# Kernel tuning notes

Hardware: AMD Instinct MI355X
Metric: run time of the kernel (lower is better)

Reference implementation:

```python
import jax, jax.numpy as jnp
import numpy as np

D_MODEL = 768
D_STATE = 16
D_CONV = 4
EXPAND = 2
D_INNER = EXPAND * D_MODEL  # 1536
DT_RANK = -(-D_MODEL // 16)  # ceil(768/16) = 48
BATCH = 1
SEQ = 2048


def _silu(v):
    return v * jax.nn.sigmoid(v)


def setup_inputs() -> dict:
    key = jax.random.key(0)
    ks = jax.random.split(key, 8)
    s = 0.02
    x = jax.random.normal(ks[0], (BATCH, SEQ, D_MODEL), jnp.float32)
    in_proj_w = jax.random.normal(ks[1], (2 * D_INNER, D_MODEL), jnp.float32) * s
    conv_w = jax.random.normal(ks[2], (D_INNER, 1, D_CONV), jnp.float32) * s  # depthwise, groups=D_INNER
    conv_b = jnp.zeros((D_INNER,), jnp.float32)
    x_proj_w = jax.random.normal(ks[3], (DT_RANK + 2 * D_STATE, D_INNER), jnp.float32) * s
    dt_proj_w = jax.random.normal(ks[4], (D_INNER, DT_RANK), jnp.float32) * s
    dt_proj_b = jax.random.normal(ks[5], (D_INNER,), jnp.float32) * 0.01
    # A = repeat_interleave(arange(1, d_state+1), d_inner rows); A_log = log(A)
    A_log = jnp.log(jnp.tile(jnp.arange(1, D_STATE + 1, dtype=jnp.float32)[None, :], (D_INNER, 1)))
    D = jnp.ones((D_INNER,), jnp.float32)
    out_proj_w = jax.random.normal(ks[6], (D_MODEL, D_INNER), jnp.float32) * s
    return {"x": x, "in_proj_w": in_proj_w, "conv_w": conv_w, "conv_b": conv_b,
            "x_proj_w": x_proj_w, "dt_proj_w": dt_proj_w, "dt_proj_b": dt_proj_b,
            "A_log": A_log, "D": D, "out_proj_w": out_proj_w}


def reference(x, in_proj_w, conv_w, conv_b, x_proj_w, dt_proj_w, dt_proj_b, A_log, D, out_proj_w):
    b, L, d = x.shape
    # in_proj then split into x-branch and gate z
    xz = x @ in_proj_w.T                       # (b, L, 2*d_inner)
    xh, z = jnp.split(xz, 2, axis=-1)          # each (b, L, d_inner)
    # causal depthwise conv1d: torch pads d_conv-1 both sides then slices [:L];
    # equivalent to left-pad d_conv-1, right-pad 0
    xc = jnp.transpose(xh, (0, 2, 1))          # (b, d_inner, L)
    xc = jax.lax.conv_general_dilated(
        xc, conv_w, window_strides=(1,), padding=[(D_CONV - 1, 0)],
        feature_group_count=D_INNER, dimension_numbers=("NCH", "OIH", "NCH"))
    xc = xc + conv_b[None, :, None]
    u = _silu(jnp.transpose(xc, (0, 2, 1)))    # (b, L, d_inner)
    # input-dependent dt, B, C
    x_dbl = u @ x_proj_w.T                     # (b, L, dt_rank + 2*d_state)
    dt, Bm, Cm = jnp.split(x_dbl, [DT_RANK, DT_RANK + D_STATE], axis=-1)
    dt = jax.nn.softplus(dt @ dt_proj_w.T + dt_proj_b)  # (b, L, d_inner)
    A = -jnp.exp(A_log)                        # (d_inner, d_state)
    # selective scan via cumprod/cumsum (faithful to source math)
    dA = jnp.exp(dt[..., None] * A[None, None])              # (b, L, d_inner, d_state)
    dBu = dt[..., None] * Bm[:, :, None, :] * u[..., None]   # (b, L, d_inner, d_state)
    p = jnp.cumprod(dA, axis=1)
    eps = jnp.finfo(u.dtype).eps
    p_safe = jnp.maximum(p, eps)
    g = jnp.cumsum(dBu / p_safe, axis=1)
    h = g * p
    y = jnp.sum(h * Cm[:, :, None, :], axis=-1) + D * u      # (b, L, d_inner)
    y = y * _silu(z)
    return y @ out_proj_w.T                    # (b, L, d_model); dropout=identity (eval)
```

## Files before the change

kernel.cpp:

```cpp
#include <hip/hip_runtime.h>
#include <hip/hip_bf16.h>

#define LSEQ 2048
#define DMODEL 768
#define DINNER 1536
#define DSTATE 16
#define DTRANK 48
#define XDBL_W (DTRANK + 2*DSTATE)
#define CHUNK 32
#define NCHUNK (LSEQ / CHUNK)
#define NDN (DINNER * DSTATE)
#define FEPS 1.1920928955078125e-07f
#define SPLITK 8
#define OSPLIT 4
#define LDST2 36

typedef short bf16x8 __attribute__((ext_vector_type(8)));
typedef float f32x4 __attribute__((ext_vector_type(4)));
typedef unsigned short u16;

__device__ __forceinline__ u16 f2bf_rn(float f) {
    unsigned u = __float_as_uint(f);
    unsigned r = u + 0x7FFFu + ((u >> 16) & 1u);
    return (u16)(r >> 16);
}
__device__ __forceinline__ float bf2f(u16 h) {
    return __uint_as_float(((unsigned)h) << 16);
}

template<int CTRL>
__device__ __forceinline__ float qperm(float x) {
    return __int_as_float(__builtin_amdgcn_update_dpp(
        0, __float_as_int(x), CTRL, 0xF, 0xF, true));
}

__global__ __launch_bounds__(256) void cvt_all(
    const float* __restrict__ w_in,  u16* __restrict__ wihi, u16* __restrict__ wilo, int n1,
    const float* __restrict__ w_out, u16* __restrict__ owhi, u16* __restrict__ owlo, int n2,
    const float* __restrict__ x,     u16* __restrict__ xhi,  u16* __restrict__ xlo)
{
    int i4 = (blockIdx.x * 256 + threadIdx.x) * 4;
    const float* src; u16* hi; u16* lo; int off;
    if (i4 < n1)            { src = w_in;  hi = wihi; lo = wilo; off = i4; }
    else if (i4 < n1 + n2)  { src = w_out; hi = owhi; lo = owlo; off = i4 - n1; }
    else                    { src = x;     hi = xhi;  lo = xlo;  off = i4 - n1 - n2; }
    float4 v = *(const float4*)&src[off];
    u16 h0 = f2bf_rn(v.x), h1 = f2bf_rn(v.y), h2 = f2bf_rn(v.z), h3 = f2bf_rn(v.w);
    u16 l0 = f2bf_rn(v.x - bf2f(h0));
    u16 l1 = f2bf_rn(v.y - bf2f(h1));
    u16 l2 = f2bf_rn(v.z - bf2f(h2));
    u16 l3 = f2bf_rn(v.w - bf2f(h3));
    *(ushort4*)&hi[off] = make_ushort4(h0, h1, h2, h3);
    *(ushort4*)&lo[off] = make_ushort4(l0, l1, l2, l3);
}

template<int BN>
__global__ __launch_bounds__(256) void mfma_gemm_tn(
    const u16* __restrict__ Ahi, const u16* __restrict__ Alo,
    const u16* __restrict__ Bhi, const u16* __restrict__ Blo,
    float* __restrict__ C, int ldc, int ldk, int Klen)
{
    constexpr int BUFSZ = 8192 + BN * 64;
    constexpr int NJ = BN / 32;
    __shared__ u16 lds[2 * BUFSZ];
    const int tid = threadIdx.x;
    const int wid = tid >> 6;
    const int lane = tid & 63;

    int nwg = gridDim.x * gridDim.y * gridDim.z;
    int lin = (blockIdx.z * gridDim.y + blockIdx.y) * gridDim.x + blockIdx.x;
    int q = nwg >> 3;
    int swz = (lin & 7) * q + (lin >> 3);
    int bx = swz % gridDim.x;
    int tmp = swz / gridDim.x;
    int by = tmp % gridDim.y;
    int bz = tmp / gridDim.y;

    const int m0 = bx * 128;
    const int n0 = by * BN;
    const int Koff = bz * Klen;

    const int st_subrow = lane >> 2;
    const int st_cphys = lane & 3;
    const u16* myplane = (wid == 0) ? Ahi : (wid == 1) ? Alo : (wid == 2) ? Bhi : Blo;
    const int rowbase = (wid < 2) ? m0 : n0;
    const int nIss = (wid < 2) ? 8 : (BN / 16);
    const int planeOff = (wid < 2) ? wid * 4096 : 8192 + (wid - 2) * (BN * 32);

    f32x4 acc[4][NJ] = {};
    const int wm = (wid >> 1) * 64;
    const int wn = (wid & 1) * (BN / 2);
    const int fr = lane & 15;
    const int fc = lane >> 4;
    const int nsteps = Klen / 32;

    auto stage = [&](int buf, int k0) {
#pragma unroll
        for (int j = 0; j < 8; ++j) {
            if (j < nIss) {
                int row = j * 16 + st_subrow;
                int clog = st_cphys ^ ((row >> 1) & 3);
                const u16* g = myplane + (size_t)(rowbase + row) * ldk + k0 + clog * 8;
                u16* l = &lds[buf * BUFSZ + planeOff + j * 512];
                __builtin_amdgcn_global_load_lds(
                    (const __attribute__((address_space(1))) unsigned int*)g,
                    (__attribute__((address_space(3))) unsigned int*)l, 16, 0, 0);
            }
        }
    };

    stage(0, Koff);
    int cur = 0;
    for (int t = 0; t < nsteps; ++t) {
        __syncthreads();
        if (t + 1 < nsteps) stage(cur ^ 1, Koff + (t + 1) * 32);

        bf16x8 ah[4], al[4], bh[NJ], bl[NJ];
        const bf16x8* L = (const bf16x8*)&lds[cur * BUFSZ];
#pragma unroll
        for (int mi = 0; mi < 4; ++mi) {
            int r = wm + mi * 16 + fr;
            int idx = r * 4 + (fc ^ ((r >> 1) & 3));
            ah[mi] = L[idx];
            al[mi] = L[512 + idx];
        }
#pragma unroll
        for (int nj = 0; nj < NJ; ++nj) {
            int r = wn + nj * 16 + fr;
            int idx = r * 4 + (fc ^ ((r >> 1) & 3));
            bh[nj] = L[1024 + idx];
            bl[nj] = L[1024 + BN * 4 + idx];
        }
#pragma unroll
        for (int mi = 0; mi < 4; ++mi)
#pragma unroll
            for (int nj = 0; nj < NJ; ++nj) {
                acc[mi][nj] = __builtin_amdgcn_mfma_f32_16x16x32_bf16(ah[mi], bh[nj], acc[mi][nj], 0, 0, 0);
                acc[mi][nj] = __builtin_amdgcn_mfma_f32_16x16x32_bf16(ah[mi], bl[nj], acc[mi][nj], 0, 0, 0);
                acc[mi][nj] = __builtin_amdgcn_mfma_f32_16x16x32_bf16(al[mi], bh[nj], acc[mi][nj], 0, 0, 0);
            }
        cur ^= 1;
    }

    float* Cz = C + (size_t)bz * LSEQ * ldc;
#pragma unroll
    for (int mi = 0; mi < 4; ++mi) {
        int row_b = m0 + wm + mi * 16 + (lane >> 4) * 4;
#pragma unroll
        for (int nj = 0; nj < NJ; ++nj) {
            int col = n0 + wn + nj * 16 + (lane & 15);
#pragma unroll
            for (int r = 0; r < 4; ++r)
                Cz[(size_t)(row_b + r) * ldc + col] = acc[mi][nj][r];
        }
    }
}

__global__ __launch_bounds__(256) void reduce4(
    const float* __restrict__ Ppart, float* __restrict__ out, int n)
{
    int i = (blockIdx.x * 256 + threadIdx.x) * 4;
    if (i >= n) return;
    float4 a0 = *(const float4*)&Ppart[i];
    float4 a1 = *(const float4*)&Ppart[(size_t)n + i];
    float4 a2 = *(const float4*)&Ppart[(size_t)2 * n + i];
    float4 a3 = *(const float4*)&Ppart[(size_t)3 * n + i];
    float4 r;
    r.x = ((a0.x + a1.x) + a2.x) + a3.x;
    r.y = ((a0.y + a1.y) + a2.y) + a3.y;
    r.z = ((a0.z + a1.z) + a2.z) + a3.z;
    r.w = ((a0.w + a1.w) + a2.w) + a3.w;
    *(float4*)&out[i] = r;
}

template<int EPI>
__global__ __launch_bounds__(256) void gemm_tn(
    const float* __restrict__ A, int lda,
    const float* __restrict__ B, int ldb,
    float* __restrict__ C, int ldc,
    int M, int N, int K,
    const float* __restrict__ bias)
{
    __shared__ float As[16][64 + 4];
    __shared__ float Bs[16][64 + 4];
    const int tid = threadIdx.x;
    const int m0 = blockIdx.x * 64;
    const int n0 = blockIdx.y * 64;
    const int tx = tid & 15;
    const int ty = tid >> 4;
    const int lr = tid >> 4;
    const int lc = tid & 15;
    float acc[4][4] = {};

    for (int k0 = 0; k0 < K; k0 += 16) {
        const int k = k0 + lc;
#pragma unroll
        for (int i = 0; i < 4; ++i) {
            int m = m0 + lr + i * 16;
            As[lc][lr + i * 16] = (m < M) ? A[(size_t)m * lda + k] : 0.f;
        }
#pragma unroll
        for (int i = 0; i < 4; ++i) {
            int n = n0 + lr + i * 16;
            Bs[lc][lr + i * 16] = (n < N) ? B[(size_t)n * ldb + k] : 0.f;
        }
        __syncthreads();
#pragma unroll
        for (int kk = 0; kk < 16; ++kk) {
            float a[4], b[4];
#pragma unroll
            for (int i = 0; i < 4; ++i) a[i] = As[kk][ty * 4 + i];
#pragma unroll
            for (int j = 0; j < 4; ++j) b[j] = Bs[kk][tx * 4 + j];
#pragma unroll
            for (int i = 0; i < 4; ++i)
#pragma unroll
                for (int j = 0; j < 4; ++j)
                    acc[i][j] = fmaf(a[i], b[j], acc[i][j]);
        }
        __syncthreads();
    }

#pragma unroll
    for (int i = 0; i < 4; ++i) {
        int m = m0 + ty * 4 + i;
        if (m >= M) continue;
#pragma unroll
        for (int j = 0; j < 4; ++j) {
            int n = n0 + tx * 4 + j;
            if (n >= N) continue;
            float v = acc[i][j];
            if (EPI == 1) {
                v += bias[n];
                v = fmaxf(v, 0.f) + log1pf(expf(-fabsf(v)));
            }
            C[(size_t)m * ldc + n] = v;
        }
    }
}

__global__ __launch_bounds__(256) void gemm_tn_splitk(
    const float* __restrict__ A, int lda,
    const float* __restrict__ B, int ldb,
    float* __restrict__ Cpart, int ldc,
    int M, int N, int Kchunk)
{
    __shared__ float As[16][64 + 4];
    __shared__ float Bs[16][64 + 4];
    const int tid = threadIdx.x;
    const int m0 = blockIdx.x * 64;
    const int n0 = blockIdx.y * 64;
    const int kb = blockIdx.z * Kchunk;
    const int tx = tid & 15;
    const int ty = tid >> 4;
    const int lr = tid >> 4;
    const int lc = tid & 15;
    float acc[4][4] = {};

    for (int k0 = kb; k0 < kb + Kchunk; k0 += 16) {
        const int k = k0 + lc;
#pragma unroll
        for (int i = 0; i < 4; ++i) {
            int m = m0 + lr + i * 16;
            As[lc][lr + i * 16] = (m < M) ? A[(size_t)m * lda + k] : 0.f;
        }
#pragma unroll
        for (int i = 0; i < 4; ++i) {
            int n = n0 + lr + i * 16;
            Bs[lc][lr + i * 16] = (n < N) ? B[(size_t)n * ldb + k] : 0.f;
        }
        __syncthreads();
#pragma unroll
        for (int kk = 0; kk < 16; ++kk) {
            float a[4], b[4];
#pragma unroll
            for (int i = 0; i < 4; ++i) a[i] = As[kk][ty * 4 + i];
#pragma unroll
            for (int j = 0; j < 4; ++j) b[j] = Bs[kk][tx * 4 + j];
#pragma unroll
            for (int i = 0; i < 4; ++i)
#pragma unroll
                for (int j = 0; j < 4; ++j)
                    acc[i][j] = fmaf(a[i], b[j], acc[i][j]);
        }
        __syncthreads();
    }

    float* Cs = Cpart + (size_t)blockIdx.z * M * ldc;
#pragma unroll
    for (int i = 0; i < 4; ++i) {
        int m = m0 + ty * 4 + i;
        if (m >= M) continue;
#pragma unroll
        for (int j = 0; j < 4; ++j) {
            int n = n0 + tx * 4 + j;
            if (n >= N) continue;
            Cs[(size_t)m * ldc + n] = acc[i][j];
        }
    }
}

__global__ __launch_bounds__(256) void splitk_reduce(
    const float* __restrict__ Ppart, float* __restrict__ out, int n)
{
    int i = blockIdx.x * 256 + threadIdx.x;
    if (i >= n) return;
    float s = 0.f;
#pragma unroll
    for (int z = 0; z < SPLITK; ++z) s += Ppart[(size_t)z * n + i];
    out[i] = s;
}

__global__ __launch_bounds__(256) void conv_silu_kernel(
    const float* __restrict__ xz,
    const float* __restrict__ conv_w,
    const float* __restrict__ conv_b,
    float* __restrict__ u)
{
    int idx = blockIdx.x * 256 + threadIdx.x;
    int d = idx % DINNER;
    int t0 = (idx / DINNER) * 4;
    float w[4];
#pragma unroll
    for (int j = 0; j < 4; ++j) w[j] = conv_w[d * 4 + j];
    const float b = conv_b[d];
    float xv[7];
#pragma unroll
    for (int k = 0; k < 7; ++k) {
        int s = t0 - 3 + k;
        xv[k] = (s >= 0) ? xz[(size_t)s * (2 * DINNER) + d] : 0.f;
    }
#pragma unroll
    for (int i = 0; i < 4; ++i) {
        float acc = b;
#pragma unroll
        for (int j = 0; j < 4; ++j)
            acc = fmaf(xv[i + j], w[j], acc);
        float sig = 1.f / (1.f + __expf(-acc));
        u[(size_t)(t0 + i) * DINNER + d] = acc * sig;
    }
}

__global__ __launch_bounds__(256) void dt_chunksum(
    const float* __restrict__ dtm, float* __restrict__ csum)
{
    int d = blockIdx.x * 256 + threadIdx.x;
    int c = blockIdx.y;
    size_t base = (size_t)c * CHUNK * DINNER + d;
    float s = 0.f;
#pragma unroll
    for (int i = 0; i < CHUNK; ++i)
        s += dtm[base + (size_t)i * DINNER];
    csum[(size_t)c * DINNER + d] = s;
}

__global__ __launch_bounds__(256) void cumdt_excl(float* __restrict__ csum)
{
    int d = blockIdx.x * 256 + threadIdx.x;
    float v[NCHUNK];
#pragma unroll
    for (int c = 0; c < NCHUNK; ++c)
        v[c] = csum[(size_t)c * DINNER + d];
    float run = 0.f;
#pragma unroll
    for (int c = 0; c < NCHUNK; ++c) {
        float t = v[c];
        v[c] = run;
        run += t;
    }
#pragma unroll
    for (int c = 0; c < NCHUNK; ++c)
        csum[(size_t)c * DINNER + d] = v[c];
}

template<int PROD>
__global__ __launch_bounds__(256) void scan_exclusive(float* __restrict__ buf)
{
    const int dn = blockIdx.x * 256 + threadIdx.x;
    float v[NCHUNK];
#pragma unroll
    for (int c = 0; c < NCHUNK; ++c)
        v[c] = buf[(size_t)c * NDN + dn];
    float run = PROD ? 1.f : 0.f;
#pragma unroll
    for (int c = 0; c < NCHUNK; ++c) {
        float t = v[c];
        v[c] = run;
        run = PROD ? run * t : run + t;
    }
#pragma unroll
    for (int c = 0; c < NCHUNK; ++c)
        buf[(size_t)c * NDN + dn] = v[c];
}

__global__ __launch_bounds__(256) void scan_chunksum(
    const float* __restrict__ dtm,
    const float* __restrict__ u,
    const float* __restrict__ xdbl,
    const float* __restrict__ A_log,
    const float* __restrict__ cumdt,
    float* __restrict__ S)
{
    __shared__ float sdtT[16][LDST2], sduT[16][LDST2], sBT[16][LDST2];
    const int tid = threadIdx.x;
    const int d0 = blockIdx.x * 16;
    const int t0 = blockIdx.y * CHUNK;
    const int r = tid >> 4, c = tid & 15;
#pragma unroll
    for (int i = 0; i < 2; ++i) {
        int t = r + i * 16;
        size_t row = (size_t)(t0 + t);
        float dtv = dtm[row * DINNER + d0 + c];
        sdtT[c][t] = dtv;
        sduT[c][t] = dtv * u[row * DINNER + d0 + c];
        sBT[c][t]  = xdbl[row * XDBL_W + DTRANK + c];
    }
    __syncthreads();
    const int n = tid & 15, dl = tid >> 4;
    const float Acoef = -expf(A_log[(d0 + dl) * DSTATE + n]);
    float s = cumdt[(size_t)blockIdx.y * DINNER + d0 + dl];
    float acc = 0.f;
#pragma unroll
    for (int tb = 0; tb < CHUNK / 4; ++tb) {
        f32x4 dq  = *(const f32x4*)&sdtT[dl][tb * 4];
        f32x4 duq = *(const f32x4*)&sduT[dl][tb * 4];
        f32x4 bq  = *(const f32x4*)&sBT[n][tb * 4];
#pragma unroll
        for (int j = 0; j < 4; ++j) {
            s += dq[j];
            float p = __expf(Acoef * s);
            acc += __fdividef(duq[j] * bq[j], fmaxf(p, FEPS));
        }
    }
    S[(size_t)blockIdx.y * NDN + d0 * DSTATE + tid] = acc;
}

__global__ __launch_bounds__(256) void scan_final(
    const float* __restrict__ dtm,
    const float* __restrict__ u,
    const float* __restrict__ xdbl,
    const float* __restrict__ A_log,
    const float* __restrict__ cumdt,
    const float* __restrict__ Gpre,
    float* __restrict__ xz)
{
    __shared__ float sdtT[64][LDST2], sduT[64][LDST2];
    __shared__ float sBT[16][LDST2], sCT[16][LDST2];
    const int tid = threadIdx.x;
    const int d0 = blockIdx.x * 64;
    const int t0 = blockIdx.y * CHUNK;

#pragma unroll
    for (int i = 0; i < 8; ++i) {
        int idx = i * 256 + tid;
        int dl = idx & 63, tl = idx >> 6;
        size_t row = (size_t)(t0 + tl);
        float dtv = dtm[row * DINNER + d0 + dl];
        sdtT[dl][tl] = dtv;
        sduT[dl][tl] = dtv * u[row * DINNER + d0 + dl];
    }
#pragma unroll
    for (int i = 0; i < 2; ++i) {
        int idx = i * 256 + tid;
        int n = idx & 15, tl = idx >> 4;
        size_t row = (size_t)(t0 + tl);
        sBT[n][tl] = xdbl[row * XDBL_W + DTRANK + n];
        sCT[n][tl] = xdbl[row * XDBL_W + DTRANK + DSTATE + n];
    }
    __syncthreads();

    const int lane = tid & 63, wid = tid >> 6;
    const int dloc = wid * 16 + (lane >> 2);
    const int d = d0 + dloc;
    const int nq = lane & 3;

    f32x4 Ar = *(const f32x4*)&A_log[d * DSTATE + nq * 4];
    float Ac[4] = {-expf(Ar[0]), -expf(Ar[1]), -expf(Ar[2]), -expf(Ar[3])};
    size_t pgbase = (size_t)blockIdx.y * NDN + (size_t)d * DSTATE + nq * 4;
    f32x4 g = *(const f32x4*)&Gpre[pgbase];
    float s = cumdt[(size_t)blockIdx.y * DINNER + d];

#pragma unroll
    for (int tb = 0; tb < CHUNK / 4; ++tb) {
        f32x4 dq  = *(const f32x4*)&sdtT[dloc][tb * 4];
        f32x4 duq = *(const f32x4*)&sduT[dloc][tb * 4];
        f32x4 b0 = *(const f32x4*)&sBT[nq * 4 + 0][tb * 4];
        f32x4 b1 = *(const f32x4*)&sBT[nq * 4 + 1][tb * 4];
        f32x4 b2 = *(const f32x4*)&sBT[nq * 4 + 2][tb * 4];
        f32x4 b3 = *(const f32x4*)&sBT[nq * 4 + 3][tb * 4];
        f32x4 c0 = *(const f32x4*)&sCT[nq * 4 + 0][tb * 4];
        f32x4 c1 = *(const f32x4*)&sCT[nq * 4 + 1][tb * 4];
        f32x4 c2 = *(const f32x4*)&sCT[nq * 4 + 2][tb * 4];
        f32x4 c3 = *(const f32x4*)&sCT[nq * 4 + 3][tb * 4];
#pragma unroll
        for (int j = 0; j < 4; ++j) {
            float duv = duq[j];
            s += dq[j];
            float p0 = __expf(Ac[0] * s);
            float p1 = __expf(Ac[1] * s);
            float p2 = __expf(Ac[2] * s);
            float p3 = __expf(Ac[3] * s);
            g[0] += __fdividef(duv * b0[j], fmaxf(p0, FEPS));
            g[1] += __fdividef(duv * b1[j], fmaxf(p1, FEPS));
            g[2] += __fdividef(duv * b2[j], fmaxf(p2, FEPS));
            g[3] += __fdividef(duv * b3[j], fmaxf(p3, FEPS));
            float part = (g[0] * p0) * c0[j];
            part = fmaf(g[1] * p1, c1[j], part);
            part = fmaf(g[2] * p2, c2[j], part);
            part = fmaf(g[3] * p3, c3[j], part);
            part += qperm<0xB1>(part);
            part += qperm<0x4E>(part);
            if (nq == 0)
                xz[(size_t)(t0 + tb * 4 + j) * (2 * DINNER) + d] = part;
        }
    }
}

__global__ __launch_bounds__(256) void gate_kernel(
    const float* __restrict__ xz,
    const float* __restrict__ u,
    const float* __restrict__ Dvec,
    u16* __restrict__ yhi, u16* __restrict__ ylo)
{
    int i4 = (blockIdx.x * 256 + threadIdx.x) * 4;
    if (i4 >= LSEQ * DINNER) return;
    int t = i4 / DINNER;
    int d = i4 - t * DINNER;
    size_t base = (size_t)t * (2 * DINNER) + d;
    float4 part = *(const float4*)&xz[base];
    float4 zv   = *(const float4*)&xz[base + DINNER];
    float4 uv   = *(const float4*)&u[i4];
    float4 Dd   = *(const float4*)&Dvec[d];
    float pa[4] = {part.x, part.y, part.z, part.w};
    float za[4] = {zv.x, zv.y, zv.z, zv.w};
    float ua[4] = {uv.x, uv.y, uv.z, uv.w};
    float Da[4] = {Dd.x, Dd.y, Dd.z, Dd.w};
    u16 ha[4], la[4];
#pragma unroll
    for (int j = 0; j < 4; ++j) {
        float sig = 1.f / (1.f + __expf(-za[j]));
        float yv = (pa[j] + Da[j] * ua[j]) * (za[j] * sig);
        ha[j] = f2bf_rn(yv);
        la[j] = f2bf_rn(yv - bf2f(ha[j]));
    }
    *(ushort4*)&yhi[i4] = make_ushort4(ha[0], ha[1], ha[2], ha[3]);
    *(ushort4*)&ylo[i4] = make_ushort4(la[0], la[1], la[2], la[3]);
}

extern "C" void kernel_launch(void* const* d_in, const int* in_sizes, int n_in,
                              void* d_out, int out_size, void* d_ws, size_t ws_size,
                              hipStream_t stream) {
    const float* x          = (const float*)d_in[0];
    const float* in_proj_w  = (const float*)d_in[1];
    const float* conv_w     = (const float*)d_in[2];
    const float* conv_b     = (const float*)d_in[3];
    const float* x_proj_w   = (const float*)d_in[4];
    const float* dt_proj_w  = (const float*)d_in[5];
    const float* dt_proj_b  = (const float*)d_in[6];
    const float* A_log      = (const float*)d_in[7];
    const float* Dvec       = (const float*)d_in[8];
    const float* out_proj_w = (const float*)d_in[9];
    float* out = (float*)d_out;

    char* w = (char*)d_ws;
    auto alloc = [&](size_t bytes) { char* p = w; w += (bytes + 255) & ~(size_t)255; return p; };

    float* xz    = (float*)alloc((size_t)LSEQ * 2 * DINNER * 4);
    float* u     = (float*)alloc((size_t)LSEQ * DINNER * 4);
    float* xdbl  = (float*)alloc((size_t)LSEQ * XDBL_W * 4);
    float* dtb   = (float*)alloc((size_t)LSEQ * DINNER * 4);
    float* csum  = (float*)alloc((size_t)NCHUNK * DINNER * 4);
    float* S     = (float*)alloc((size_t)NCHUNK * NDN * 4);
    float* Ppart = (float*)alloc((size_t)SPLITK * LSEQ * XDBL_W * 4);
    u16* xhi  = (u16*)alloc((size_t)LSEQ * DMODEL * 2);
    u16* xlo  = (u16*)alloc((size_t)LSEQ * DMODEL * 2);
    u16* wihi = (u16*)alloc((size_t)2 * DINNER * DMODEL * 2);
    u16* wilo = (u16*)alloc((size_t)2 * DINNER * DMODEL * 2);
    u16* owhi = (u16*)alloc((size_t)DMODEL * DINNER * 2);
    u16* owlo = (u16*)alloc((size_t)DMODEL * DINNER * 2);
    u16* yhi  = (u16*)alloc((size_t)LSEQ * DINNER * 2);
    u16* ylo  = (u16*)alloc((size_t)LSEQ * DINNER * 2);
    float* opart = u;

    dim3 blk(256);

    {
        int n1 = 2 * DINNER * DMODEL;
        int n2 = DMODEL * DINNER;
        int n3 = LSEQ * DMODEL;
        cvt_all<<<(n1 + n2 + n3) / 1024, blk, 0, stream>>>(
            in_proj_w, wihi, wilo, n1, out_proj_w, owhi, owlo, n2, x, xhi, xlo);
    }

    mfma_gemm_tn<128><<<dim3(LSEQ / 128, (2 * DINNER) / 128, 1), blk, 0, stream>>>(
        xhi, xlo, wihi, wilo, xz, 2 * DINNER, DMODEL, DMODEL);

    conv_silu_kernel<<<(LSEQ / 4) * DINNER / 256, blk, 0, stream>>>(xz, conv_w, conv_b, u);

    gemm_tn_splitk<<<dim3(LSEQ / 64, (XDBL_W + 63) / 64, SPLITK), blk, 0, stream>>>(
        u, DINNER, x_proj_w, DINNER, Ppart, XDBL_W, LSEQ, XDBL_W, DINNER / SPLITK);
    splitk_reduce<<<(LSEQ * XDBL_W + 255) / 256, blk, 0, stream>>>(Ppart, xdbl, LSEQ * XDBL_W);

    gemm_tn<1><<<dim3(LSEQ / 64, DINNER / 64), blk, 0, stream>>>(
        xdbl, XDBL_W, dt_proj_w, DTRANK, dtb, DINNER, LSEQ, DINNER, DTRANK, dt_proj_b);

    dt_chunksum<<<dim3(DINNER / 256, NCHUNK), blk, 0, stream>>>(dtb, csum);
    cumdt_excl<<<DINNER / 256, blk, 0, stream>>>(csum);
    scan_chunksum<<<dim3(DINNER / 16, NCHUNK), blk, 0, stream>>>(dtb, u, xdbl, A_log, csum, S);
    scan_exclusive<0><<<NDN / 256, blk, 0, stream>>>(S);
    scan_final<<<dim3(DINNER / 64, NCHUNK), blk, 0, stream>>>(
        dtb, u, xdbl, A_log, csum, S, xz);

    gate_kernel<<<(LSEQ * DINNER) / 1024, blk, 0, stream>>>(xz, u, Dvec, yhi, ylo);

    mfma_gemm_tn<64><<<dim3(LSEQ / 128, DMODEL / 64, OSPLIT), blk, 0, stream>>>(
        yhi, ylo, owhi, owlo, opart, DMODEL, DINNER, DINNER / OSPLIT);
    reduce4<<<(LSEQ * DMODEL) / 1024, blk, 0, stream>>>(opart, out, LSEQ * DMODEL);
}
```

Baseline: 215.2 us.

## Fuse fp32-to-bf16 hi/lo split into GEMM tile loading, drop cvt_all kernel

Removes the standalone conversion kernel that split x, in_proj_w and out_proj_w into bf16 hi/lo planes. The MFMA GEMM now loads fp32 tiles into registers, converts them to hi/lo bf16 and writes them to LDS, with loads for the next step issued before the MFMA work and LDS writes after it. This saves one launch and the extra global traffic of the pre-converted planes. In exchange, weights are re-converted by every tile that reads them, fp32 loads move twice the bytes, and async global_load_lds is replaced by register staging that adds VGPR pressure.

```diff
diff --git a/kernel.cpp b/kernel.cpp
--- a/kernel.cpp
+++ b/kernel.cpp
@@ -34,34 +34,26 @@
         0, __float_as_int(x), CTRL, 0xF, 0xF, true));
 }
 
-__global__ __launch_bounds__(256) void cvt_all(
-    const float* __restrict__ w_in,  u16* __restrict__ wihi, u16* __restrict__ wilo, int n1,
-    const float* __restrict__ w_out, u16* __restrict__ owhi, u16* __restrict__ owlo, int n2,
-    const float* __restrict__ x,     u16* __restrict__ xhi,  u16* __restrict__ xlo)
-{
-    int i4 = (blockIdx.x * 256 + threadIdx.x) * 4;
-    const float* src; u16* hi; u16* lo; int off;
-    if (i4 < n1)            { src = w_in;  hi = wihi; lo = wilo; off = i4; }
-    else if (i4 < n1 + n2)  { src = w_out; hi = owhi; lo = owlo; off = i4 - n1; }
-    else                    { src = x;     hi = xhi;  lo = xlo;  off = i4 - n1 - n2; }
-    float4 v = *(const float4*)&src[off];
-    u16 h0 = f2bf_rn(v.x), h1 = f2bf_rn(v.y), h2 = f2bf_rn(v.z), h3 = f2bf_rn(v.w);
-    u16 l0 = f2bf_rn(v.x - bf2f(h0));
-    u16 l1 = f2bf_rn(v.y - bf2f(h1));
-    u16 l2 = f2bf_rn(v.z - bf2f(h2));
-    u16 l3 = f2bf_rn(v.w - bf2f(h3));
-    *(ushort4*)&hi[off] = make_ushort4(h0, h1, h2, h3);
-    *(ushort4*)&lo[off] = make_ushort4(l0, l1, l2, l3);
-}
-
-template<int BN>
+__device__ __forceinline__ void cvt8(float4 v0, float4 v1, bf16x8& h, bf16x8& l) {
+    float f[8] = {v0.x, v0.y, v0.z, v0.w, v1.x, v1.y, v1.z, v1.w};
+#pragma unroll
+    for (int i = 0; i < 8; ++i) {
+        u16 hh = f2bf_rn(f[i]);
+        h[i] = (short)hh;
+        l[i] = (short)f2bf_rn(f[i] - bf2f(hh));
+    }
+}
+
+template<int BN, bool AU16>
 __global__ __launch_bounds__(256) void mfma_gemm_tn(
+    const float* __restrict__ Af32,
     const u16* __restrict__ Ahi, const u16* __restrict__ Alo,
-    const u16* __restrict__ Bhi, const u16* __restrict__ Blo,
+    const float* __restrict__ Bf32,
     float* __restrict__ C, int ldc, int ldk, int Klen)
 {
     constexpr int BUFSZ = 8192 + BN * 64;
     constexpr int NJ = BN / 32;
+    constexpr int NBJ = (BN * 4) / 256;
     __shared__ u16 lds[2 * BUFSZ];
     const int tid = threadIdx.x;
     const int wid = tid >> 6;
@@ -82,10 +74,6 @@
 
     const int st_subrow = lane >> 2;
     const int st_cphys = lane & 3;
-    const u16* myplane = (wid == 0) ? Ahi : (wid == 1) ? Alo : (wid == 2) ? Bhi : Blo;
-    const int rowbase = (wid < 2) ? m0 : n0;
-    const int nIss = (wid < 2) ? 8 : (BN / 16);
-    const int planeOff = (wid < 2) ? wid * 4096 : 8192 + (wid - 2) * (BN * 32);
 
     f32x4 acc[4][NJ] = {};
     const int wm = (wid >> 1) * 64;
@@ -94,26 +82,78 @@
     const int fc = lane >> 4;
     const int nsteps = Klen / 32;
 
-    auto stage = [&](int buf, int k0) {
-#pragma unroll
-        for (int j = 0; j < 8; ++j) {
-            if (j < nIss) {
-                int row = j * 16 + st_subrow;
-                int clog = st_cphys ^ ((row >> 1) & 3);
-                const u16* g = myplane + (size_t)(rowbase + row) * ldk + k0 + clog * 8;
-                u16* l = &lds[buf * BUFSZ + planeOff + j * 512];
-                __builtin_amdgcn_global_load_lds(
-                    (const __attribute__((address_space(1))) unsigned int*)g,
-                    (__attribute__((address_space(3))) unsigned int*)l, 16, 0, 0);
+    float4 aRaw[2][2];
+    float4 bRaw[NBJ][2];
+
+    auto issue_loads = [&](int buf, int k0) {
+        if (AU16) {
+            if (wid < 2) {
+                const u16* myplane = (wid == 0) ? Ahi : Alo;
+                const int planeOff = wid * 4096;
+#pragma unroll
+                for (int j = 0; j < 8; ++j) {
+                    int row = j * 16 + st_subrow;
+                    int clog = st_cphys ^ ((row >> 1) & 3);
+                    const u16* g = myplane + (size_t)(m0 + row) * ldk + k0 + clog * 8;
+                    u16* l = &lds[buf * BUFSZ + planeOff + j * 512];
+                    __builtin_amdgcn_global_load_lds(
+                        (const __attribute__((address_space(1))) unsigned int*)g,
+                        (__attribute__((address_space(3))) unsigned int*)l, 16, 0, 0);
+                }
             }
+        } else {
+#pragma unroll
+            for (int ju = 0; ju < 2; ++ju) {
+                int u = tid + 256 * ju;
+                int row = u >> 2, gc = u & 3;
+                const float* g = Af32 + (size_t)(m0 + row) * ldk + k0 + gc * 8;
+                aRaw[ju][0] = *(const float4*)g;
+                aRaw[ju][1] = *(const float4*)(g + 4);
+            }
+        }
+#pragma unroll
+        for (int ju = 0; ju < NBJ; ++ju) {
+            int u = tid + 256 * ju;
+            int row = u >> 2, gc = u & 3;
+            const float* g = Bf32 + (size_t)(n0 + row) * ldk + k0 + gc * 8;
+            bRaw[ju][0] = *(const float4*)g;
+            bRaw[ju][1] = *(const float4*)(g + 4);
         }
     };
 
-    stage(0, Koff);
+    auto write_regs = [&](int buf) {
+        bf16x8* Lw = (bf16x8*)&lds[buf * BUFSZ];
+        if (!AU16) {
+#pragma unroll
+            for (int ju = 0; ju < 2; ++ju) {
+                int u = tid + 256 * ju;
+                int row = u >> 2, gc = u & 3;
+                int du = row * 4 + (gc ^ ((row >> 1) & 3));
+                bf16x8 h, l;
+                cvt8(aRaw[ju][0], aRaw[ju][1], h, l);
+                Lw[du] = h;
+                Lw[512 + du] = l;
+            }
+        }
+#pragma unroll
+        for (int ju = 0; ju < NBJ; ++ju) {
+            int u = tid + 256 * ju;
+            int row = u >> 2, gc = u & 3;
+            int du = row * 4 + (gc ^ ((row >> 1) & 3));
+            bf16x8 h, l;
+            cvt8(bRaw[ju][0], bRaw[ju][1], h, l);
+            Lw[1024 + du] = h;
+            Lw[1024 + BN * 4 + du] = l;
+        }
+    };
+
+    issue_loads(0, Koff);
+    write_regs(0);
+    __syncthreads();
+
     int cur = 0;
     for (int t = 0; t < nsteps; ++t) {
-        __syncthreads();
-        if (t + 1 < nsteps) stage(cur ^ 1, Koff + (t + 1) * 32);
+        if (t + 1 < nsteps) issue_loads(cur ^ 1, Koff + (t + 1) * 32);
 
         bf16x8 ah[4], al[4], bh[NJ], bl[NJ];
         const bf16x8* L = (const bf16x8*)&lds[cur * BUFSZ];
@@ -139,6 +179,9 @@
                 acc[mi][nj] = __builtin_amdgcn_mfma_f32_16x16x32_bf16(ah[mi], bl[nj], acc[mi][nj], 0, 0, 0);
                 acc[mi][nj] = __builtin_amdgcn_mfma_f32_16x16x32_bf16(al[mi], bh[nj], acc[mi][nj], 0, 0, 0);
             }
+
+        if (t + 1 < nsteps) write_regs(cur ^ 1);
+        __syncthreads();
         cur ^= 1;
     }
 
@@ -572,28 +615,14 @@
     float* csum  = (float*)alloc((size_t)NCHUNK * DINNER * 4);
     float* S     = (float*)alloc((size_t)NCHUNK * NDN * 4);
     float* Ppart = (float*)alloc((size_t)SPLITK * LSEQ * XDBL_W * 4);
-    u16* xhi  = (u16*)alloc((size_t)LSEQ * DMODEL * 2);
-    u16* xlo  = (u16*)alloc((size_t)LSEQ * DMODEL * 2);
-    u16* wihi = (u16*)alloc((size_t)2 * DINNER * DMODEL * 2);
-    u16* wilo = (u16*)alloc((size_t)2 * DINNER * DMODEL * 2);
-    u16* owhi = (u16*)alloc((size_t)DMODEL * DINNER * 2);
-    u16* owlo = (u16*)alloc((size_t)DMODEL * DINNER * 2);
     u16* yhi  = (u16*)alloc((size_t)LSEQ * DINNER * 2);
     u16* ylo  = (u16*)alloc((size_t)LSEQ * DINNER * 2);
     float* opart = u;
 
     dim3 blk(256);
 
-    {
-        int n1 = 2 * DINNER * DMODEL;
-        int n2 = DMODEL * DINNER;
-        int n3 = LSEQ * DMODEL;
-        cvt_all<<<(n1 + n2 + n3) / 1024, blk, 0, stream>>>(
-            in_proj_w, wihi, wilo, n1, out_proj_w, owhi, owlo, n2, x, xhi, xlo);
-    }
-
-    mfma_gemm_tn<128><<<dim3(LSEQ / 128, (2 * DINNER) / 128, 1), blk, 0, stream>>>(
-        xhi, xlo, wihi, wilo, xz, 2 * DINNER, DMODEL, DMODEL);
+    mfma_gemm_tn<128, false><<<dim3(LSEQ / 128, (2 * DINNER) / 128, 1), blk, 0, stream>>>(
+        x, nullptr, nullptr, in_proj_w, xz, 2 * DINNER, DMODEL, DMODEL);
 
     conv_silu_kernel<<<(LSEQ / 4) * DINNER / 256, blk, 0, stream>>>(xz, conv_w, conv_b, u);
 
@@ -613,7 +642,7 @@
 
     gate_kernel<<<(LSEQ * DINNER) / 1024, blk, 0, stream>>>(xz, u, Dvec, yhi, ylo);
 
-    mfma_gemm_tn<64><<<dim3(LSEQ / 128, DMODEL / 64, OSPLIT), blk, 0, stream>>>(
-        yhi, ylo, owhi, owlo, opart, DMODEL, DINNER, DINNER / OSPLIT);
+    mfma_gemm_tn<64, true><<<dim3(LSEQ / 128, DMODEL / 64, OSPLIT), blk, 0, stream>>>(
+        nullptr, yhi, ylo, out_proj_w, opart, DMODEL, DINNER, DINNER / OSPLIT);
     reduce4<<<(LSEQ * DMODEL) / 1024, blk, 0, stream>>>(opart, out, LSEQ * DMODEL);
 }
```

After: 221.9 us. 1.03x slower.
